# Kernel tuning notes

Hardware: AMD Instinct MI355X
Metric: run time of the kernel (lower is better)

Reference implementation:

```python
import jax, jax.numpy as jnp
import numpy as np

B, C, D, H, W = 4, 64, 32, 64, 64
S, NH = 8, 4
HD = C // NH


def setup_inputs() -> dict:
    key = jax.random.key(0)
    ks = jax.random.split(key, 8)
    sc = 0.05
    return {
        "x": jax.random.normal(ks[0], (B, C, D, H, W), jnp.float32),
        "slot_init": jax.random.normal(ks[1], (1, C, S), jnp.float32),
        "slot_proj_w": jax.random.normal(ks[2], (C, C), jnp.float32) * sc,
        "slot_proj_b": jnp.zeros((C,), jnp.float32),
        "ln_g": jnp.ones((C,), jnp.float32),
        "ln_b": jnp.zeros((C,), jnp.float32),
        "in_proj_w": jax.random.normal(ks[3], (3 * C, C), jnp.float32) * sc,
        "in_proj_b": jnp.zeros((3 * C,), jnp.float32),
        "out_proj_w": jax.random.normal(ks[4], (C, C), jnp.float32) * sc,
        "out_proj_b": jnp.zeros((C,), jnp.float32),
        "feat_w": jax.random.normal(ks[5], (C, C), jnp.float32) * sc,
        "feat_b": jnp.zeros((C,), jnp.float32),
        "s2f_w": jax.random.normal(ks[6], (C, C), jnp.float32) * sc,
        "s2f_b": jnp.zeros((C,), jnp.float32),
    }


def _l2norm(v, axis):
    # F.normalize: v / max(||v||, eps)
    n = jnp.sqrt(jnp.sum(v * v, axis=axis, keepdims=True))
    return v / jnp.maximum(n, 1e-12)


def reference(x, slot_init, slot_proj_w, slot_proj_b, ln_g, ln_b,
              in_proj_w, in_proj_b, out_proj_w, out_proj_b,
              feat_w, feat_b, s2f_w, s2f_b):
    b, c, d, h, w = x.shape
    n = d * h * w
    x_flat = x.reshape(b, c, n)                                  # (b,c,N)
    slots = jnp.broadcast_to(slot_init, (b, c, S))               # (b,c,S)

    # ---- slot update: cosine-sim cross attention over N ----
    x_norm = _l2norm(x_flat, 1)
    slots_norm = _l2norm(slots, 1)
    sim = jnp.einsum('bcs,bcn->bsn', slots_norm, x_norm)         # (b,S,N)
    attn = jax.nn.softmax(sim, axis=2)
    updates = jnp.einsum('bcn,bsn->bsc', x_flat, attn)           # (b,S,c)
    slots_t = updates @ slot_proj_w.T + slot_proj_b              # (b,S,c)

    # ---- LayerNorm(channels) then tiny MHSA over S=8 slots ----
    mu = jnp.mean(slots_t, axis=-1, keepdims=True)
    var = jnp.mean((slots_t - mu) ** 2, axis=-1, keepdims=True)
    sn = (slots_t - mu) / jnp.sqrt(var + 1e-5) * ln_g + ln_b     # (b,S,c)

    qkv = sn @ in_proj_w.T + in_proj_b                           # (b,S,3c)
    q, k, v = jnp.split(qkv, 3, axis=-1)
    def heads(t):
        return t.reshape(b, S, NH, HD).transpose(0, 2, 1, 3)     # (b,H,S,hd)
    q, k, v = heads(q), heads(k), heads(v)
    scores = jnp.einsum('bhqd,bhkd->bhqk', q, k) / jnp.sqrt(jnp.float32(HD))
    a = jax.nn.softmax(scores, axis=-1)
    o = jnp.einsum('bhqk,bhkd->bhqd', a, v).transpose(0, 2, 1, 3).reshape(b, S, c)
    o = o @ out_proj_w.T + out_proj_b
    slots_t = slots_t + o                                        # (b,S,c)

    # ---- feature broadcast: 1x1x1 conv + slot->feature attention ----
    feat_flat = jnp.einsum('oc,bcn->bon', feat_w, x_flat) + feat_b[None, :, None]
    slots_feat = slots_t @ s2f_w.T + s2f_b                       # (b,S,c)
    sim2 = jnp.einsum('bsc,bcn->bsn', slots_feat, feat_flat)
    attn2 = jax.nn.softmax(sim2, axis=1)                         # softmax over slots
    out = jnp.einsum('bsc,bsn->bcn', slots_t, attn2)             # (b,c,N)
    return out.reshape(b, c, d, h, w) + x
```

## Files before the change

kernel.cpp:

```cpp
#include <hip/hip_runtime.h>
#include <hip/hip_bf16.h>

#define BB   4
#define CC   64
#define SS   8
#define NN   (32*64*64)
#define NH_  4
#define HD_  16
#define TA   128
#define BPA  128
#define NTB  8

typedef __attribute__((ext_vector_type(8))) short bf16x8;
typedef __attribute__((ext_vector_type(4))) float f32x4;

__device__ __forceinline__ unsigned short f2b(float f) {
    union { float f; unsigned u; } v; v.f = f;
    unsigned r = v.u + 0x7FFFu + ((v.u >> 16) & 1u);
    return (unsigned short)(r >> 16);
}
__device__ __forceinline__ unsigned bfpack(float a, float b) {
    union { float f; unsigned u; } x, y; x.f = a; y.f = b;
    unsigned ra = (x.u + 0x7FFFu + ((x.u >> 16) & 1u)) >> 16;
    unsigned rb = (y.u + 0x7FFFu + ((y.u >> 16) & 1u)) & 0xFFFF0000u;
    return ra | rb;
}

__global__ __launch_bounds__(256) void k_precomp(
    const float* __restrict__ slot_init,
    const float* __restrict__ s2fw, const float* __restrict__ s2fb,
    const float* __restrict__ fw, const float* __restrict__ fb,
    float* __restrict__ M, float* __restrict__ g0v,
    float* __restrict__ hv, float* __restrict__ h0,
    float* __restrict__ snT_ws)
{
    const int tid = threadIdx.x;
    if (blockIdx.x < 16) {
        const int cp = blockIdx.x*4 + (tid >> 6);
        const int c  = tid & 63;
        float acc = 0.f;
        #pragma unroll 8
        for (int o = 0; o < CC; ++o)
            acc += s2fw[o*CC + cp] * fw[o*CC + c];
        M[cp*CC + c] = acc;
    } else if (blockIdx.x == 16) {
        if (tid < 64) {
            float acc = 0.f;
            #pragma unroll 8
            for (int o = 0; o < CC; ++o) acc += s2fb[o] * fw[o*CC + tid];
            g0v[tid] = acc;
        } else if (tid < 128) {
            const int cp = tid - 64;
            float acc = 0.f;
            #pragma unroll 8
            for (int o = 0; o < CC; ++o) acc += s2fw[o*CC + cp] * fb[o];
            hv[cp] = acc;
        } else if (tid == 128) {
            float acc = 0.f;
            for (int o = 0; o < CC; ++o) acc += s2fb[o] * fb[o];
            *h0 = acc;
        }
    } else {
        __shared__ float nrm[SS];
        if (tid < 64) {
            const int s = tid & 7, ch = tid >> 3;
            float p = 0.f;
            #pragma unroll
            for (int j = 0; j < 8; ++j) {
                float v = slot_init[(ch*8 + j)*SS + s];
                p += v*v;
            }
            p += __shfl_xor(p, 8); p += __shfl_xor(p, 16); p += __shfl_xor(p, 32);
            if (tid < 8) nrm[s] = fmaxf(sqrtf(p), 1e-12f);
        }
        __syncthreads();
        for (int i = tid; i < SS*CC; i += 256) {
            const int c = i >> 3, s = i & 7;
            snT_ws[i] = slot_init[c*SS + s] / nrm[s];
        }
    }
}

__global__ __launch_bounds__(256) void k_slots_attn(
    const float* __restrict__ x, const float* __restrict__ snT_ws,
    float* __restrict__ U_part, float* __restrict__ sume_part)
{
    __shared__ float xlds[2][CC * TA];
    __shared__ short et[9 * TA];
    __shared__ float snT[CC * SS];

    const int tid = threadIdx.x;
    const int b   = blockIdx.x / BPA;
    const int blk = blockIdx.x % BPA;
    const int lane = tid & 63, wv = tid >> 6;
    const int col = tid >> 1, half = tid & 1;

    if (tid < 64) ((int*)&et[8*TA])[tid] = 0;
    if (tid < 128) *(float4*)&snT[tid*4] = *(const float4*)&snT_ws[tid*4];

    const float* xb = x + (size_t)b * CC * NN;

    f32x4 accU = {0.f, 0.f, 0.f, 0.f};
    float accS[4];
    #pragma unroll
    for (int j = 0; j < 4; ++j) accS[j] = 0.f;

    #define STAGE(buf, t)                                                      \
    {                                                                          \
        const int n0_ = (t) * TA;                                              \
        _Pragma("unroll")                                                      \
        for (int k = 0; k < 8; ++k) {                                          \
            const int c_  = (wv*8 + k)*2 + (lane >> 5);                        \
            const int jg_ = (lane & 31) ^ (c_ & 7);                            \
            const float* src_ = xb + (size_t)c_*NN + n0_ + jg_*4;              \
            float* dst_ = &xlds[buf][(wv*8 + k)*256];                          \
            __builtin_amdgcn_global_load_lds(                                  \
                (const __attribute__((address_space(1))) void*)src_,           \
                (__attribute__((address_space(3))) void*)dst_, 16, 0, 0);      \
        }                                                                      \
    }

    int cur = 0;
    STAGE(0, blk);
    asm volatile("s_waitcnt vmcnt(0)" ::: "memory");
    __syncthreads();

    for (int tt = 0; tt < NTB; ++tt) {
        if (tt + 1 < NTB) STAGE(cur ^ 1, blk + (tt+1)*BPA);

        {
            const float* xl = &xlds[cur][0];
            float ss = 0.f;
            float a[SS];
            #pragma unroll
            for (int s = 0; s < SS; ++s) a[s] = 0.f;
            #pragma unroll
            for (int ci = 0; ci < 32; ++ci) {
                const int c = half*32 + ci;
                const float xv = xl[c*TA + (((col>>2) ^ (c&7)) << 2) + (col&3)];
                ss += xv * xv;
                const float4 g0 = *(const float4*)&snT[c*8];
                const float4 g1 = *(const float4*)&snT[c*8 + 4];
                a[0] += g0.x*xv; a[1] += g0.y*xv; a[2] += g0.z*xv; a[3] += g0.w*xv;
                a[4] += g1.x*xv; a[5] += g1.y*xv; a[6] += g1.z*xv; a[7] += g1.w*xv;
            }
            ss += __shfl_xor(ss, 1);
            #pragma unroll
            for (int s = 0; s < SS; ++s) a[s] += __shfl_xor(a[s], 1);

            const float invn = 1.f / fmaxf(sqrtf(ss), 1e-12f);
            #pragma unroll
            for (int j = 0; j < 4; ++j) {
                const int s = half*4 + j;
                const float e = __expf(a[s] * invn);
                accS[j] += e;
                et[s*TA + ((((col>>3) ^ s) << 3) | (col & 7))] = (short)f2b(e);
            }
        }
        __syncthreads();

        {
            const int ca  = (wv << 4) + (lane & 15);
            const int rbq = lane & 15;
            const int rb  = (rbq < 8) ? rbq : 8;
            const int p   = lane >> 4;
            #pragma unroll
            for (int kk = 0; kk < 4; ++kk) {
                const int n8  = kk*32 + p*8;
                const int sl0 = ((n8 >> 2)     ^ (ca & 7));
                const int sl1 = (((n8 >> 2)+1) ^ (ca & 7));
                const float4 f0 = *(const float4*)&xlds[cur][ca*TA + sl0*4];
                const float4 f1 = *(const float4*)&xlds[cur][ca*TA + sl1*4];
                union { unsigned u[4]; bf16x8 v; } ua;
                ua.u[0] = bfpack(f0.x, f0.y);
                ua.u[1] = bfpack(f0.z, f0.w);
                ua.u[2] = bfpack(f1.x, f1.y);
                ua.u[3] = bfpack(f1.z, f1.w);
                const int slb = ((n8 >> 3) ^ (rb & 7));
                const bf16x8 bfr = *(const bf16x8*)&et[rb*TA + slb*8];
                accU = __builtin_amdgcn_mfma_f32_16x16x32_bf16(ua.v, bfr, accU, 0, 0, 0);
            }
        }
        asm volatile("s_waitcnt vmcnt(0)" ::: "memory");
        __syncthreads();
        cur ^= 1;
    }

    {
        const size_t base = ((size_t)(b*BPA + blk) * SS) * CC;
        if ((lane & 15) < SS) {
            const int s  = lane & 15;
            const int c0 = (wv << 4) + ((lane >> 4) << 2);
            #pragma unroll
            for (int r = 0; r < 4; ++r)
                U_part[base + s*CC + c0 + r] = accU[r];
        }
    }
    {
        float* scratch = &xlds[0][0];
        #pragma unroll
        for (int j = 0; j < 4; ++j)
            scratch[(half*4 + j)*TA + col] = accS[j];
        __syncthreads();
        const int s = tid >> 5, k = tid & 31;
        float v = 0.f;
        #pragma unroll
        for (int i = 0; i < 4; ++i) v += scratch[s*TA + k*4 + i];
        v += __shfl_xor(v, 1); v += __shfl_xor(v, 2); v += __shfl_xor(v, 4);
        v += __shfl_xor(v, 8); v += __shfl_xor(v, 16);
        if (k == 0) sume_part[(size_t)(b*BPA + blk)*SS + s] = v;
    }
    #undef STAGE
}

__global__ __launch_bounds__(256) void k_reduce2(
    const float* __restrict__ U_part, const float* __restrict__ sume_part,
    float* __restrict__ upd_g, int bpb)
{
    __shared__ float part[4][64];
    __shared__ float lbuf[256];
    __shared__ float Lsh;
    const int tid = threadIdx.x;
    const int b = blockIdx.x >> 3, s = blockIdx.x & 7;
    const int c = tid & 63, kc = tid >> 6;
    const int cnt = bpb >> 2;

    float lv = 0.f;
    for (int k = tid; k < bpb; k += 256)
        lv += sume_part[(size_t)(b*bpb + k)*SS + s];
    lbuf[tid] = lv;

    float acc[8];
    #pragma unroll
    for (int j = 0; j < 8; ++j) acc[j] = 0.f;
    const float* base = U_part + ((size_t)(b*bpb + kc*cnt)*SS + s)*CC + c;
    for (int k = 0; k < cnt; k += 8) {
        #pragma unroll
        for (int j = 0; j < 8; ++j)
            acc[j] += base[(size_t)(k + j) * SS * CC];
    }
    part[kc][c] = ((acc[0]+acc[1]) + (acc[2]+acc[3]))
                + ((acc[4]+acc[5]) + (acc[6]+acc[7]));
    __syncthreads();

    if (tid < 128) lbuf[tid] += lbuf[tid + 128];
    __syncthreads();
    if (tid < 64) {
        float v = lbuf[tid] + lbuf[tid + 64];
        v += __shfl_xor(v, 1); v += __shfl_xor(v, 2); v += __shfl_xor(v, 4);
        v += __shfl_xor(v, 8); v += __shfl_xor(v, 16); v += __shfl_xor(v, 32);
        if (tid == 0) Lsh = v;
    }
    __syncthreads();

    if (tid < 64) {
        float u = part[0][c] + part[1][c] + part[2][c] + part[3][c];
        upd_g[((size_t)b*SS + s)*CC + c] = u / Lsh;
    }
}

__global__ __launch_bounds__(256) void k_slots_small(
    const float* __restrict__ upd_g,
    const float* __restrict__ spw, const float* __restrict__ spb,
    const float* __restrict__ lng, const float* __restrict__ lnb,
    const float* __restrict__ ipw, const float* __restrict__ ipb,
    const float* __restrict__ opw, const float* __restrict__ opb,
    const float* __restrict__ M, const float* __restrict__ g0v,
    const float* __restrict__ hv, const float* __restrict__ h0,
    float* __restrict__ st_out, float* __restrict__ g_out, float* __restrict__ h_out)
{
    __shared__ float upd[SS*CC];
    __shared__ float st [SS*CC];
    __shared__ float snb[SS*CC];
    __shared__ float qkv[SS*3*CC];
    __shared__ float ot [SS*CC];

    const int tid  = threadIdx.x;
    const int b    = blockIdx.x;
    const int c    = tid & 63;
    const int quad = tid >> 6;
    const int r0 = quad*2, r1 = r0 + 1;
    float wreg[CC];

    #pragma unroll
    for (int i = 0; i < 16; ++i)
        *(float4*)&wreg[i*4] = *(const float4*)(spw + c*CC + i*4);
    upd[r0*CC + c] = upd_g[(b*SS + r0)*CC + c];
    upd[r1*CC + c] = upd_g[(b*SS + r1)*CC + c];
    __syncthreads();

    {
        const float bias = spb[c];
        float a0 = bias, a1 = bias;
        #pragma unroll
        for (int i = 0; i < 16; ++i) {
            float4 u0 = *(const float4*)&upd[r0*CC + i*4];
            float4 u1 = *(const float4*)&upd[r1*CC + i*4];
            a0 += u0.x*wreg[i*4+0] + u0.y*wreg[i*4+1] + u0.z*wreg[i*4+2] + u0.w*wreg[i*4+3];
            a1 += u1.x*wreg[i*4+0] + u1.y*wreg[i*4+1] + u1.z*wreg[i*4+2] + u1.w*wreg[i*4+3];
        }
        st[r0*CC + c] = a0;
        st[r1*CC + c] = a1;
    }
    __syncthreads();

    {
        const int row = tid >> 5, l = tid & 31;
        float v0 = st[row*CC + l], v1 = st[row*CC + l + 32];
        float sum = v0 + v1;
        sum += __shfl_xor(sum, 1); sum += __shfl_xor(sum, 2); sum += __shfl_xor(sum, 4);
        sum += __shfl_xor(sum, 8); sum += __shfl_xor(sum, 16);
        const float mu = sum * (1.f/64.f);
        const float d0 = v0 - mu, d1 = v1 - mu;
        float vs = d0*d0 + d1*d1;
        vs += __shfl_xor(vs, 1); vs += __shfl_xor(vs, 2); vs += __shfl_xor(vs, 4);
        vs += __shfl_xor(vs, 8); vs += __shfl_xor(vs, 16);
        const float rstd = rsqrtf(vs * (1.f/64.f) + 1e-5f);
        snb[row*CC + l]      = d0 * rstd * lng[l]      + lnb[l];
        snb[row*CC + l + 32] = d1 * rstd * lng[l + 32] + lnb[l + 32];
    }
    __syncthreads();

    for (int m = 0; m < 3; ++m) {
        #pragma unroll
        for (int i = 0; i < 16; ++i)
            *(float4*)&wreg[i*4] = *(const float4*)(ipw + (size_t)(m*CC + c)*CC + i*4);
        const float bias = ipb[m*CC + c];
        float a0 = bias, a1 = bias;
        #pragma unroll
        for (int i = 0; i < 16; ++i) {
            float4 u0 = *(const float4*)&snb[r0*CC + i*4];
            float4 u1 = *(const float4*)&snb[r1*CC + i*4];
            a0 += u0.x*wreg[i*4+0] + u0.y*wreg[i*4+1] + u0.z*wreg[i*4+2] + u0.w*wreg[i*4+3];
            a1 += u1.x*wreg[i*4+0] + u1.y*wreg[i*4+1] + u1.z*wreg[i*4+2] + u1.w*wreg[i*4+3];
        }
        qkv[r0*3*CC + m*CC + c] = a0;
        qkv[r1*3*CC + m*CC + c] = a1;
    }
    __syncthreads();

    if (tid < NH_*SS) {
        const int h = tid >> 3, q = tid & 7;
        float qreg[HD_];
        #pragma unroll
        for (int i = 0; i < 4; ++i)
            *(float4*)&qreg[i*4] = *(const float4*)&qkv[q*3*CC + h*HD_ + i*4];
        float srow[SS];
        float mx = -1e30f;
        #pragma unroll
        for (int k = 0; k < SS; ++k) {
            float acc = 0.f;
            #pragma unroll
            for (int d = 0; d < HD_; ++d)
                acc += qreg[d] * qkv[k*3*CC + CC + h*HD_ + d];
            srow[k] = acc * 0.25f;
            mx = fmaxf(mx, srow[k]);
        }
        float l = 0.f;
        #pragma unroll
        for (int k = 0; k < SS; ++k) { srow[k] = __expf(srow[k] - mx); l += srow[k]; }
        const float inv = 1.f / l;
        float oreg[HD_];
        #pragma unroll
        for (int d = 0; d < HD_; ++d) oreg[d] = 0.f;
        #pragma unroll
        for (int k = 0; k < SS; ++k) {
            #pragma unroll
            for (int d = 0; d < HD_; ++d)
                oreg[d] += srow[k] * qkv[k*3*CC + 2*CC + h*HD_ + d];
        }
        #pragma unroll
        for (int d = 0; d < HD_; ++d)
            ot[q*CC + h*HD_ + d] = oreg[d] * inv;
    }
    __syncthreads();

    #pragma unroll
    for (int i = 0; i < 16; ++i)
        *(float4*)&wreg[i*4] = *(const float4*)(opw + c*CC + i*4);
    {
        const float bias = opb[c];
        float a0 = bias, a1 = bias;
        #pragma unroll
        for (int i = 0; i < 16; ++i) {
            float4 u0 = *(const float4*)&ot[r0*CC + i*4];
            float4 u1 = *(const float4*)&ot[r1*CC + i*4];
            a0 += u0.x*wreg[i*4+0] + u0.y*wreg[i*4+1] + u0.z*wreg[i*4+2] + u0.w*wreg[i*4+3];
            a1 += u1.x*wreg[i*4+0] + u1.y*wreg[i*4+1] + u1.z*wreg[i*4+2] + u1.w*wreg[i*4+3];
        }
        st[r0*CC + c] += a0;
        st[r1*CC + c] += a1;
    }
    __syncthreads();

    #pragma unroll 8
    for (int cp = 0; cp < CC; ++cp) wreg[cp] = M[cp*CC + c];
    {
        const float g0 = g0v[c];
        float a0 = g0, a1 = g0;
        #pragma unroll
        for (int i = 0; i < 16; ++i) {
            float4 s0 = *(const float4*)&st[r0*CC + i*4];
            float4 s1 = *(const float4*)&st[r1*CC + i*4];
            a0 += s0.x*wreg[i*4+0] + s0.y*wreg[i*4+1] + s0.z*wreg[i*4+2] + s0.w*wreg[i*4+3];
            a1 += s1.x*wreg[i*4+0] + s1.y*wreg[i*4+1] + s1.z*wreg[i*4+2] + s1.w*wreg[i*4+3];
        }
        g_out[(b*SS + r0)*CC + c] = a0;
        g_out[(b*SS + r1)*CC + c] = a1;
        st_out[(b*SS + r0)*CC + c] = st[r0*CC + c];
        st_out[(b*SS + r1)*CC + c] = st[r1*CC + c];
    }
    {
        const int row = tid >> 5, l = tid & 31;
        float pv = st[row*CC + l]*hv[l] + st[row*CC + l + 32]*hv[l + 32];
        pv += __shfl_xor(pv, 1); pv += __shfl_xor(pv, 2); pv += __shfl_xor(pv, 4);
        pv += __shfl_xor(pv, 8); pv += __shfl_xor(pv, 16);
        if (l == 0) h_out[b*SS + row] = pv + *h0;
    }
}

__global__ __launch_bounds__(256) void k_feat(
    const float* __restrict__ x,
    const float* __restrict__ st_g, const float* __restrict__ g_g,
    const float* __restrict__ h_g,
    float* __restrict__ out)
{
    __shared__ float stS[SS*CC];
    __shared__ float gS [SS*CC];
    __shared__ float hS [SS];

    const int tid = threadIdx.x;
    const int b  = blockIdx.x >> 9;
    const int n  = ((blockIdx.x & 511) << 8) + tid;

    for (int i = tid; i < SS*CC; i += 256) {
        stS[i] = st_g[b*SS*CC + i];
        gS[i]  = g_g [b*SS*CC + i];
    }
    if (tid < SS) hS[tid] = h_g[b*SS + tid];
    __syncthreads();

    const float* xb = x + (size_t)b * CC * NN + n;
    float xc[CC];
    #pragma unroll
    for (int c = 0; c < CC; ++c) xc[c] = xb[(size_t)c * NN];

    float a[SS];
    #pragma unroll
    for (int s = 0; s < SS; ++s) a[s] = hS[s];
    #pragma unroll
    for (int c4 = 0; c4 < CC/4; ++c4) {
        #pragma unroll
        for (int s = 0; s < SS; ++s) {
            float4 g4 = *(const float4*)(&gS[s*CC + c4*4]);
            a[s] += g4.x*xc[c4*4+0] + g4.y*xc[c4*4+1]
                  + g4.z*xc[c4*4+2] + g4.w*xc[c4*4+3];
        }
    }

    float m = a[0];
    #pragma unroll
    for (int s = 1; s < SS; ++s) m = fmaxf(m, a[s]);
    float l = 0.f;
    #pragma unroll
    for (int s = 0; s < SS; ++s) { a[s] = __expf(a[s] - m); l += a[s]; }
    const float inv = 1.f / l;

    float* ob = out + (size_t)b * CC * NN + n;
    #pragma unroll
    for (int c4 = 0; c4 < CC/4; ++c4) {
        float o0 = 0.f, o1 = 0.f, o2 = 0.f, o3 = 0.f;
        #pragma unroll
        for (int s = 0; s < SS; ++s) {
            float4 s4 = *(const float4*)(&stS[s*CC + c4*4]);
            o0 += s4.x * a[s]; o1 += s4.y * a[s];
            o2 += s4.z * a[s]; o3 += s4.w * a[s];
        }
        __builtin_nontemporal_store(o0 * inv + xc[c4*4+0], ob + (size_t)(c4*4+0) * NN);
        __builtin_nontemporal_store(o1 * inv + xc[c4*4+1], ob + (size_t)(c4*4+1) * NN);
        __builtin_nontemporal_store(o2 * inv + xc[c4*4+2], ob + (size_t)(c4*4+2) * NN);
        __builtin_nontemporal_store(o3 * inv + xc[c4*4+3], ob + (size_t)(c4*4+3) * NN);
    }
}

extern "C" void kernel_launch(void* const* d_in, const int* in_sizes, int n_in,
                              void* d_out, int out_size, void* d_ws, size_t ws_size,
                              hipStream_t stream) {
    const float* x         = (const float*)d_in[0];
    const float* slot_init = (const float*)d_in[1];
    const float* spw       = (const float*)d_in[2];
    const float* spb       = (const float*)d_in[3];
    const float* lng       = (const float*)d_in[4];
    const float* lnb       = (const float*)d_in[5];
    const float* ipw       = (const float*)d_in[6];
    const float* ipb       = (const float*)d_in[7];
    const float* opw       = (const float*)d_in[8];
    const float* opb       = (const float*)d_in[9];
    const float* fw        = (const float*)d_in[10];
    const float* fb        = (const float*)d_in[11];
    const float* s2fw      = (const float*)d_in[12];
    const float* s2fb      = (const float*)d_in[13];
    float* out = (float*)d_out;

    float* w         = (float*)d_ws;
    float* U_part    = w;
    float* sume_part = U_part + (size_t)BB*BPA*SS*CC;
    float* upd_g     = sume_part + (size_t)BB*BPA*SS;
    float* Mm        = upd_g + 2048;
    float* g0v       = Mm + 4096;
    float* hv        = g0v + 64;
    float* h0        = hv + 64;
    float* snT_ws    = h0 + 64;
    float* st_out    = snT_ws + 1024;
    float* g_out     = st_out + 2048;
    float* h_out     = g_out + 2048;

    k_precomp<<<18, 256, 0, stream>>>(slot_init, s2fw, s2fb, fw, fb,
                                      Mm, g0v, hv, h0, snT_ws);
    k_slots_attn<<<BB * BPA, 256, 0, stream>>>(x, snT_ws, U_part, sume_part);
    k_reduce2<<<BB * SS, 256, 0, stream>>>(U_part, sume_part, upd_g, BPA);
    k_slots_small<<<BB, 256, 0, stream>>>(upd_g, spw, spb, lng, lnb,
                                          ipw, ipb, opw, opb, Mm, g0v, hv, h0,
                                          st_out, g_out, h_out);
    k_feat<<<BB * (NN/256), 256, 0, stream>>>(x, st_out, g_out, h_out, out);
}
```

Baseline: 128.7 us.

## Halve slot-attention tile width and double blocks per batch

The column tile in the slot-attention kernel shrinks from 128 to 64 points while the block count per batch doubles from 128 to 256. Each point's channel dot products are now split across four threads instead of two, with an extra shuffle stage. The LDS swizzle gains a higher-order XOR bit to keep bank conflicts low at the narrower row stride. This halves LDS use per block to raise occupancy and spread the pass over more blocks, at the cost of more partial results for the reduce kernel and more shuffle work per point.

```diff
diff --git a/kernel.cpp b/kernel.cpp
--- a/kernel.cpp
+++ b/kernel.cpp
@@ -7,8 +7,8 @@
 #define NN   (32*64*64)
 #define NH_  4
 #define HD_  16
-#define TA   128
-#define BPA  128
+#define TA   64
+#define BPA  256
 #define NTB  8
 
 typedef __attribute__((ext_vector_type(8))) short bf16x8;
@@ -93,27 +93,28 @@
     const int b   = blockIdx.x / BPA;
     const int blk = blockIdx.x % BPA;
     const int lane = tid & 63, wv = tid >> 6;
-    const int col = tid >> 1, half = tid & 1;
-
-    if (tid < 64) ((int*)&et[8*TA])[tid] = 0;
+    const int col = tid >> 2, q4 = tid & 3;
+
+    if (tid < 32) ((int*)&et[8*TA])[tid] = 0;
     if (tid < 128) *(float4*)&snT[tid*4] = *(const float4*)&snT_ws[tid*4];
 
     const float* xb = x + (size_t)b * CC * NN;
 
     f32x4 accU = {0.f, 0.f, 0.f, 0.f};
-    float accS[4];
-    #pragma unroll
-    for (int j = 0; j < 4; ++j) accS[j] = 0.f;
+    float accS[2];
+    accS[0] = 0.f; accS[1] = 0.f;
+
+    #define XMASK(c_) (((c_) & 7) ^ ((((c_) >> 4) & 1) << 3))
 
     #define STAGE(buf, t)                                                      \
     {                                                                          \
         const int n0_ = (t) * TA;                                              \
         _Pragma("unroll")                                                      \
-        for (int k = 0; k < 8; ++k) {                                          \
-            const int c_  = (wv*8 + k)*2 + (lane >> 5);                        \
-            const int jg_ = (lane & 31) ^ (c_ & 7);                            \
-            const float* src_ = xb + (size_t)c_*NN + n0_ + jg_*4;              \
-            float* dst_ = &xlds[buf][(wv*8 + k)*256];                          \
+        for (int k = 0; k < 4; ++k) {                                          \
+            const int c_  = wv*16 + k*4 + (lane >> 4);                         \
+            const int j_  = (lane & 15) ^ XMASK(c_);                           \
+            const float* src_ = xb + (size_t)c_*NN + n0_ + j_*4;               \
+            float* dst_ = &xlds[buf][(wv*16 + k*4)*TA];                        \
             __builtin_amdgcn_global_load_lds(                                  \
                 (const __attribute__((address_space(1))) void*)src_,           \
                 (__attribute__((address_space(3))) void*)dst_, 16, 0, 0);      \
@@ -135,23 +136,26 @@
             #pragma unroll
             for (int s = 0; s < SS; ++s) a[s] = 0.f;
             #pragma unroll
-            for (int ci = 0; ci < 32; ++ci) {
-                const int c = half*32 + ci;
-                const float xv = xl[c*TA + (((col>>2) ^ (c&7)) << 2) + (col&3)];
+            for (int ci = 0; ci < 16; ++ci) {
+                const int c = q4*16 + ci;
+                const float xv = xl[c*TA + (((col>>2) ^ XMASK(c)) << 2) + (col&3)];
                 ss += xv * xv;
                 const float4 g0 = *(const float4*)&snT[c*8];
                 const float4 g1 = *(const float4*)&snT[c*8 + 4];
                 a[0] += g0.x*xv; a[1] += g0.y*xv; a[2] += g0.z*xv; a[3] += g0.w*xv;
                 a[4] += g1.x*xv; a[5] += g1.y*xv; a[6] += g1.z*xv; a[7] += g1.w*xv;
             }
-            ss += __shfl_xor(ss, 1);
-            #pragma unroll
-            for (int s = 0; s < SS; ++s) a[s] += __shfl_xor(a[s], 1);
+            ss += __shfl_xor(ss, 1);  ss += __shfl_xor(ss, 2);
+            #pragma unroll
+            for (int s = 0; s < SS; ++s) {
+                a[s] += __shfl_xor(a[s], 1);
+                a[s] += __shfl_xor(a[s], 2);
+            }
 
             const float invn = 1.f / fmaxf(sqrtf(ss), 1e-12f);
             #pragma unroll
-            for (int j = 0; j < 4; ++j) {
-                const int s = half*4 + j;
+            for (int j = 0; j < 2; ++j) {
+                const int s = q4*2 + j;
                 const float e = __expf(a[s] * invn);
                 accS[j] += e;
                 et[s*TA + ((((col>>3) ^ s) << 3) | (col & 7))] = (short)f2b(e);
@@ -164,11 +168,12 @@
             const int rbq = lane & 15;
             const int rb  = (rbq < 8) ? rbq : 8;
             const int p   = lane >> 4;
-            #pragma unroll
-            for (int kk = 0; kk < 4; ++kk) {
+            const int am  = XMASK(ca);
+            #pragma unroll
+            for (int kk = 0; kk < 2; ++kk) {
                 const int n8  = kk*32 + p*8;
-                const int sl0 = ((n8 >> 2)     ^ (ca & 7));
-                const int sl1 = (((n8 >> 2)+1) ^ (ca & 7));
+                const int sl0 = ((n8 >> 2)     ^ am);
+                const int sl1 = (((n8 >> 2)+1) ^ am);
                 const float4 f0 = *(const float4*)&xlds[cur][ca*TA + sl0*4];
                 const float4 f1 = *(const float4*)&xlds[cur][ca*TA + sl1*4];
                 union { unsigned u[4]; bf16x8 v; } ua;
@@ -198,19 +203,17 @@
     }
     {
         float* scratch = &xlds[0][0];
-        #pragma unroll
-        for (int j = 0; j < 4; ++j)
-            scratch[(half*4 + j)*TA + col] = accS[j];
+        scratch[(q4*2 + 0)*TA + col] = accS[0];
+        scratch[(q4*2 + 1)*TA + col] = accS[1];
         __syncthreads();
         const int s = tid >> 5, k = tid & 31;
-        float v = 0.f;
-        #pragma unroll
-        for (int i = 0; i < 4; ++i) v += scratch[s*TA + k*4 + i];
+        float v = scratch[s*TA + k*2] + scratch[s*TA + k*2 + 1];
         v += __shfl_xor(v, 1); v += __shfl_xor(v, 2); v += __shfl_xor(v, 4);
         v += __shfl_xor(v, 8); v += __shfl_xor(v, 16);
         if (k == 0) sume_part[(size_t)(b*BPA + blk)*SS + s] = v;
     }
     #undef STAGE
+    #undef XMASK
 }
 
 __global__ __launch_bounds__(256) void k_reduce2(
```

Measured after the change: 146.4 us. +13.7%, slower.
